# Performance work log

Hardware: AMD Instinct MI355X
Metric: run time of the kernel (lower is better)

The kernel has to match this reference:

```python
import jax, jax.numpy as jnp
import numpy as np

D_ENC = 512
D_DEC = 512
D_JOINT = D_ENC + D_DEC  # 1024
V = 1024


def setup_inputs() -> dict:
    key = jax.random.key(0)
    ks = jax.random.split(key, 8)
    s = lambda fan_in: 1.0 / np.sqrt(fan_in)
    return {
        "encoder_output": jax.random.normal(ks[0], (8, 200, D_ENC), dtype=jnp.float32),
        "decoder_output": jax.random.normal(ks[1], (8, 50, D_DEC), dtype=jnp.float32),
        "W_enc": jax.random.uniform(ks[2], (D_JOINT, D_ENC), jnp.float32, -s(D_ENC), s(D_ENC)),
        "b_enc": jax.random.uniform(ks[3], (D_JOINT,), jnp.float32, -s(D_ENC), s(D_ENC)),
        "W_dec": jax.random.uniform(ks[4], (D_JOINT, D_DEC), jnp.float32, -s(D_DEC), s(D_DEC)),
        "b_dec": jax.random.uniform(ks[5], (D_JOINT,), jnp.float32, -s(D_DEC), s(D_DEC)),
        "W_fc": jax.random.uniform(ks[6], (V, D_JOINT), jnp.float32, -s(D_JOINT), s(D_JOINT)),
        "b_fc": jax.random.uniform(ks[7], (V,), jnp.float32, -s(D_JOINT), s(D_JOINT)),
    }


def reference(encoder_output, decoder_output, W_enc, b_enc, W_dec, b_dec, W_fc, b_fc):
    # enc: (B, T, D_JOINT); dec: (B, U, D_JOINT)
    enc = jnp.einsum('btd,jd->btj', encoder_output, W_enc) + b_enc
    dec = jnp.einsum('bud,jd->buj', decoder_output, W_dec) + b_dec
    # broadcast join: (B, T, U, D_JOINT)
    combined = enc[:, :, None, :] + dec[:, None, :, :]
    logits = jnp.einsum('btuj,vj->btuv', jnp.tanh(combined), W_fc) + b_fc
    return jax.nn.log_softmax(logits, axis=-1)
```

## Files before the change

kernel.cpp:

```cpp
#include <hip/hip_runtime.h>
#include <hip/hip_bf16.h>

#define TT 200
#define UU 50
#define BB 8
#define DJ 1024
#define DE 512
#define VV 1024
#define M_TOTAL (BB*TT*UU)
#define MB 80
#define NITER 32

typedef __bf16 bf16x8 __attribute__((ext_vector_type(8)));
typedef float f32x4 __attribute__((ext_vector_type(4)));

__device__ __forceinline__ float fast_tanh(float x) {
    float e = __expf(2.f * x);
    return 1.f - 2.f / (e + 1.f);
}

__device__ __forceinline__ bf16x8 tanh_pack8(float4 e0, float4 e1, float4 d0, float4 d1) {
    bf16x8 h;
    h[0] = (__bf16)fast_tanh(e0.x + d0.x); h[1] = (__bf16)fast_tanh(e0.y + d0.y);
    h[2] = (__bf16)fast_tanh(e0.z + d0.z); h[3] = (__bf16)fast_tanh(e0.w + d0.w);
    h[4] = (__bf16)fast_tanh(e1.x + d1.x); h[5] = (__bf16)fast_tanh(e1.y + d1.y);
    h[6] = (__bf16)fast_tanh(e1.z + d1.z); h[7] = (__bf16)fast_tanh(e1.w + d1.w);
    return h;
}

__device__ __forceinline__ void gload_lds16(const unsigned short* g, unsigned short* l) {
    __builtin_amdgcn_global_load_lds(
        (const __attribute__((address_space(1))) unsigned int*)(const void*)g,
        (__attribute__((address_space(3))) unsigned int*)(void*)l, 16, 0, 0);
}

__global__ void k_wfct(const float* __restrict__ w, unsigned short* __restrict__ o) {
    const int G = blockIdx.x * 256 + threadIdx.x;
    const int gk = G >> 10, n = G & 1023;
    const float* src = w + (size_t)n * DJ + gk * 8;
    float4 a = *(const float4*)(src);
    float4 b = *(const float4*)(src + 4);
    bf16x8 h;
    h[0] = (__bf16)a.x; h[1] = (__bf16)a.y; h[2] = (__bf16)a.z; h[3] = (__bf16)a.w;
    h[4] = (__bf16)b.x; h[5] = (__bf16)b.y; h[6] = (__bf16)b.z; h[7] = (__bf16)b.w;
    *(bf16x8*)(o + (size_t)G * 8) = h;
}

__global__ __launch_bounds__(256) void k_proj2(const float* __restrict__ enc,
                                               const float* __restrict__ dec,
                                               const float* __restrict__ W_enc,
                                               const float* __restrict__ b_enc,
                                               const float* __restrict__ W_dec,
                                               const float* __restrict__ b_dec,
                                               float* __restrict__ encp,
                                               float* __restrict__ decp) {
    __shared__ float in_s[16][DE];
    const bool isDec = blockIdx.x >= 100;
    const float* in  = isDec ? dec   : enc;
    const float* W   = isDec ? W_dec : W_enc;
    const float* bia = isDec ? b_dec : b_enc;
    float* out       = isDec ? decp  : encp;
    const int m0 = (isDec ? (blockIdx.x - 100) : blockIdx.x) * 16;
    const int tid = threadIdx.x;
    #pragma unroll
    for (int it = 0; it < 8; ++it) {
        int idx = tid + it * 256;
        int r = idx >> 7, c = (idx & 127) << 2;
        *(float4*)&in_s[r][c] = *(const float4*)(in + (size_t)(m0 + r) * DE + c);
    }
    __syncthreads();
    const int j = blockIdx.y * 256 + tid;
    const float4* wr = (const float4*)(W + (size_t)j * DE);
    float acc[16];
    #pragma unroll
    for (int r = 0; r < 16; ++r) acc[r] = 0.f;
    for (int d4 = 0; d4 < DE / 4; ++d4) {
        float4 w = wr[d4];
        #pragma unroll
        for (int r = 0; r < 16; ++r) {
            float4 x = *(const float4*)&in_s[r][d4 << 2];
            acc[r] += x.x * w.x + x.y * w.y + x.z * w.z + x.w * w.w;
        }
    }
    float bv = bia[j];
    #pragma unroll
    for (int r = 0; r < 16; ++r)
        out[(size_t)(m0 + r) * DJ + j] = acc[r] + bv;
}

__global__ __launch_bounds__(512, 2) void k_joint(const float* __restrict__ encp,
                                                  const float* __restrict__ decp,
                                                  const unsigned short* __restrict__ wfcg,
                                                  const float* __restrict__ bfc,
                                                  float* __restrict__ out) {
    __shared__ unsigned short Bs[2][4096 * 8];
    __shared__ unsigned short As[2][320 * 8];
    __shared__ float red[8][MB];

    const int tid = threadIdx.x;
    const int wave = tid >> 6, lane = tid & 63;
    const int g = lane >> 4, ln = lane & 15;
    const int bid = blockIdx.x;
    const int m0 = bid * MB;

    const bool aRole = (tid < 320);
    const float *er = encp, *dr = decp;
    int agran = 0;
    if (aRole) {
        const int m = tid % MB;
        const int gk = tid / MB;
        const int mrow = m0 + m;
        const int b = mrow / (TT * UU);
        const int rem = mrow - b * (TT * UU);
        const int t = rem / UU;
        const int u = rem - t * UU;
        er = encp + (size_t)(b * TT + t) * DJ + gk * 8;
        dr = decp + (size_t)(b * UU + u) * DJ + gk * 8;
        agran = gk * MB + m;
    }

    f32x4 acc[5][8];
    #pragma unroll
    for (int mf = 0; mf < 5; ++mf)
        #pragma unroll
        for (int nf = 0; nf < 8; ++nf)
            acc[mf][nf] = (f32x4){0.f, 0.f, 0.f, 0.f};

    {
        const int kb0 = bid & 31;
        if (aRole) {
            const int ko = kb0 * 32;
            float4 e0 = *(const float4*)(er + ko);
            float4 e1 = *(const float4*)(er + ko + 4);
            float4 d0 = *(const float4*)(dr + ko);
            float4 d1 = *(const float4*)(dr + ko + 4);
            *(bf16x8*)&As[0][agran * 8] = tanh_pack8(e0, e1, d0, d1);
        }
        const unsigned short* src = wfcg + (size_t)kb0 * 4096 * 8;
        #pragma unroll
        for (int r = 0; r < 8; ++r)
            gload_lds16(src + (size_t)(r * 512 + tid) * 8, &Bs[0][(r * 512 + wave * 64) * 8]);
    }
    __syncthreads();

    for (int it = 0; it < NITER; ++it) {
        const int cur = it & 1, nxt = cur ^ 1;
        const bool notlast = (it < NITER - 1);
        float4 e0, e1, d0, d1;
        if (notlast) {
            const int kb = (it + 1 + bid) & 31;
            if (aRole) {
                const int ko = kb * 32;
                e0 = *(const float4*)(er + ko);
                e1 = *(const float4*)(er + ko + 4);
                d0 = *(const float4*)(dr + ko);
                d1 = *(const float4*)(dr + ko + 4);
            }
            const unsigned short* src = wfcg + (size_t)kb * 4096 * 8;
            #pragma unroll
            for (int r = 0; r < 8; ++r)
                gload_lds16(src + (size_t)(r * 512 + tid) * 8, &Bs[nxt][(r * 512 + wave * 64) * 8]);
        }
        bf16x8 af[5];
        #pragma unroll
        for (int mf = 0; mf < 5; ++mf)
            af[mf] = *(const bf16x8*)&As[cur][(g * MB + mf * 16 + ln) * 8];
        #pragma unroll
        for (int nf = 0; nf < 8; ++nf) {
            bf16x8 bfr = *(const bf16x8*)&Bs[cur][(g * 1024 + wave * 128 + nf * 16 + ln) * 8];
            #pragma unroll
            for (int mf = 0; mf < 5; ++mf)
                acc[mf][nf] = __builtin_amdgcn_mfma_f32_16x16x32_bf16(af[mf], bfr, acc[mf][nf], 0, 0, 0);
        }
        if (notlast && aRole)
            *(bf16x8*)&As[nxt][agran * 8] = tanh_pack8(e0, e1, d0, d1);
        __syncthreads();
    }

    float bv[8];
    #pragma unroll
    for (int nf = 0; nf < 8; ++nf) bv[nf] = bfc[wave * 128 + nf * 16 + ln];
    #pragma unroll
    for (int mf = 0; mf < 5; ++mf)
        #pragma unroll
        for (int nf = 0; nf < 8; ++nf)
            #pragma unroll
            for (int j = 0; j < 4; ++j)
                acc[mf][nf][j] += bv[nf];

    float rmx[5][4];
    #pragma unroll
    for (int mf = 0; mf < 5; ++mf)
        #pragma unroll
        for (int j = 0; j < 4; ++j) {
            float mx = -3.0e38f;
            #pragma unroll
            for (int nf = 0; nf < 8; ++nf) mx = fmaxf(mx, acc[mf][nf][j]);
            #pragma unroll
            for (int s = 1; s < 16; s <<= 1) mx = fmaxf(mx, __shfl_xor(mx, s));
            rmx[mf][j] = mx;
        }
    if (ln == 0) {
        #pragma unroll
        for (int mf = 0; mf < 5; ++mf)
            #pragma unroll
            for (int j = 0; j < 4; ++j)
                red[wave][mf * 16 + g * 4 + j] = rmx[mf][j];
    }
    __syncthreads();
    #pragma unroll
    for (int mf = 0; mf < 5; ++mf)
        #pragma unroll
        for (int j = 0; j < 4; ++j) {
            const int r = mf * 16 + g * 4 + j;
            float mx = red[0][r];
            #pragma unroll
            for (int w = 1; w < 8; ++w) mx = fmaxf(mx, red[w][r]);
            rmx[mf][j] = mx;
        }
    __syncthreads();

    float rsm[5][4];
    #pragma unroll
    for (int mf = 0; mf < 5; ++mf)
        #pragma unroll
        for (int j = 0; j < 4; ++j) {
            float s = 0.f;
            #pragma unroll
            for (int nf = 0; nf < 8; ++nf) s += __expf(acc[mf][nf][j] - rmx[mf][j]);
            #pragma unroll
            for (int t2 = 1; t2 < 16; t2 <<= 1) s += __shfl_xor(s, t2);
            rsm[mf][j] = s;
        }
    if (ln == 0) {
        #pragma unroll
        for (int mf = 0; mf < 5; ++mf)
            #pragma unroll
            for (int j = 0; j < 4; ++j)
                red[wave][mf * 16 + g * 4 + j] = rsm[mf][j];
    }
    __syncthreads();
    #pragma unroll
    for (int mf = 0; mf < 5; ++mf)
        #pragma unroll
        for (int j = 0; j < 4; ++j) {
            const int r = mf * 16 + g * 4 + j;
            float s = 0.f;
            #pragma unroll
            for (int w = 0; w < 8; ++w) s += red[w][r];
            const float lse = rmx[mf][j] + __logf(s);
            float* op = out + (size_t)(m0 + r) * VV + wave * 128 + ln;
            #pragma unroll
            for (int nf = 0; nf < 8; ++nf)
                __builtin_nontemporal_store(acc[mf][nf][j] - lse, op + nf * 16);
        }
}

extern "C" void kernel_launch(void* const* d_in, const int* in_sizes, int n_in,
                              void* d_out, int out_size, void* d_ws, size_t ws_size,
                              hipStream_t stream) {
    const float* enc   = (const float*)d_in[0];
    const float* dec   = (const float*)d_in[1];
    const float* W_enc = (const float*)d_in[2];
    const float* b_enc = (const float*)d_in[3];
    const float* W_dec = (const float*)d_in[4];
    const float* b_dec = (const float*)d_in[5];
    const float* W_fc  = (const float*)d_in[6];
    const float* b_fc  = (const float*)d_in[7];
    float* out = (float*)d_out;

    float* encp = (float*)d_ws;
    float* decp = encp + (size_t)BB * TT * DJ;
    unsigned short* wfcg = (unsigned short*)(decp + (size_t)BB * UU * DJ);

    k_wfct<<<(VV * DJ) / (256 * 8), 256, 0, stream>>>(W_fc, wfcg);
    k_proj2<<<dim3(125, DJ / 256), 256, 0, stream>>>(enc, dec, W_enc, b_enc, W_dec, b_dec, encp, decp);
    k_joint<<<M_TOTAL / MB, 512, 0, stream>>>(encp, decp, wfcg, b_fc, out);
}
```

Measured before the change: 404.1 us.

## Switch joint GEMM to FP8 MFMA with scaled weights and triple-buffered LDS

Converts the W_fc weights (pre-scaled by 32) and the tanh activations to FP8 e4m3, and runs the joint GEMM with fp8 MFMA instead of bf16. The scale is removed in the epilogue before the bias is added. This halves LDS and global traffic per K-step and uses the higher-rate FP8 matrix instructions. The double buffer becomes a three-stage LDS ring with manual s_waitcnt plus barrier, and the MFMA section runs at raised wave priority. The cost is lower precision in the logits, which may approach the accuracy tolerance.

```diff
diff --git a/kernel.cpp b/kernel.cpp
--- a/kernel.cpp
+++ b/kernel.cpp
@@ -1,5 +1,6 @@
 #include <hip/hip_runtime.h>
 #include <hip/hip_bf16.h>
+#include <hip/hip_fp8.h>
 
 #define TT 200
 #define UU 50
@@ -10,8 +11,8 @@
 #define M_TOTAL (BB*TT*UU)
 #define MB 80
 #define NITER 32
-
-typedef __bf16 bf16x8 __attribute__((ext_vector_type(8)));
+#define WINV (1.0f/32.0f)
+
 typedef float f32x4 __attribute__((ext_vector_type(4)));
 
 __device__ __forceinline__ float fast_tanh(float x) {
@@ -19,31 +20,45 @@
     return 1.f - 2.f / (e + 1.f);
 }
 
-__device__ __forceinline__ bf16x8 tanh_pack8(float4 e0, float4 e1, float4 d0, float4 d1) {
-    bf16x8 h;
-    h[0] = (__bf16)fast_tanh(e0.x + d0.x); h[1] = (__bf16)fast_tanh(e0.y + d0.y);
-    h[2] = (__bf16)fast_tanh(e0.z + d0.z); h[3] = (__bf16)fast_tanh(e0.w + d0.w);
-    h[4] = (__bf16)fast_tanh(e1.x + d1.x); h[5] = (__bf16)fast_tanh(e1.y + d1.y);
-    h[6] = (__bf16)fast_tanh(e1.z + d1.z); h[7] = (__bf16)fast_tanh(e1.w + d1.w);
-    return h;
-}
-
-__device__ __forceinline__ void gload_lds16(const unsigned short* g, unsigned short* l) {
+__device__ __forceinline__ unsigned char f2fp8(float x) {
+    return __hip_fp8_e4m3(x).__x;
+}
+
+__device__ __forceinline__ unsigned long long tanh_pack_fp8(float4 e0, float4 e1, float4 d0, float4 d1) {
+    unsigned long long r;
+    r  = (unsigned long long)f2fp8(fast_tanh(e0.x + d0.x));
+    r |= (unsigned long long)f2fp8(fast_tanh(e0.y + d0.y)) << 8;
+    r |= (unsigned long long)f2fp8(fast_tanh(e0.z + d0.z)) << 16;
+    r |= (unsigned long long)f2fp8(fast_tanh(e0.w + d0.w)) << 24;
+    r |= (unsigned long long)f2fp8(fast_tanh(e1.x + d1.x)) << 32;
+    r |= (unsigned long long)f2fp8(fast_tanh(e1.y + d1.y)) << 40;
+    r |= (unsigned long long)f2fp8(fast_tanh(e1.z + d1.z)) << 48;
+    r |= (unsigned long long)f2fp8(fast_tanh(e1.w + d1.w)) << 56;
+    return r;
+}
+
+__device__ __forceinline__ void gload_lds16(const unsigned char* g, unsigned char* l) {
     __builtin_amdgcn_global_load_lds(
         (const __attribute__((address_space(1))) unsigned int*)(const void*)g,
         (__attribute__((address_space(3))) unsigned int*)(void*)l, 16, 0, 0);
 }
 
-__global__ void k_wfct(const float* __restrict__ w, unsigned short* __restrict__ o) {
+__global__ void k_wfct(const float* __restrict__ w, unsigned char* __restrict__ o) {
     const int G = blockIdx.x * 256 + threadIdx.x;
     const int gk = G >> 10, n = G & 1023;
     const float* src = w + (size_t)n * DJ + gk * 8;
     float4 a = *(const float4*)(src);
     float4 b = *(const float4*)(src + 4);
-    bf16x8 h;
-    h[0] = (__bf16)a.x; h[1] = (__bf16)a.y; h[2] = (__bf16)a.z; h[3] = (__bf16)a.w;
-    h[4] = (__bf16)b.x; h[5] = (__bf16)b.y; h[6] = (__bf16)b.z; h[7] = (__bf16)b.w;
-    *(bf16x8*)(o + (size_t)G * 8) = h;
+    unsigned long long r;
+    r  = (unsigned long long)f2fp8(a.x * 32.f);
+    r |= (unsigned long long)f2fp8(a.y * 32.f) << 8;
+    r |= (unsigned long long)f2fp8(a.z * 32.f) << 16;
+    r |= (unsigned long long)f2fp8(a.w * 32.f) << 24;
+    r |= (unsigned long long)f2fp8(b.x * 32.f) << 32;
+    r |= (unsigned long long)f2fp8(b.y * 32.f) << 40;
+    r |= (unsigned long long)f2fp8(b.z * 32.f) << 48;
+    r |= (unsigned long long)f2fp8(b.w * 32.f) << 56;
+    *(unsigned long long*)(o + (size_t)G * 8) = r;
 }
 
 __global__ __launch_bounds__(256) void k_proj2(const float* __restrict__ enc,
@@ -90,11 +105,11 @@
 
 __global__ __launch_bounds__(512, 2) void k_joint(const float* __restrict__ encp,
                                                   const float* __restrict__ decp,
-                                                  const unsigned short* __restrict__ wfcg,
+                                                  const unsigned char* __restrict__ wfc8,
                                                   const float* __restrict__ bfc,
                                                   float* __restrict__ out) {
-    __shared__ unsigned short Bs[2][4096 * 8];
-    __shared__ unsigned short As[2][320 * 8];
+    __shared__ unsigned char Bs[3][32768];
+    __shared__ unsigned char As[3][2560];
     __shared__ float red[8][MB];
 
     const int tid = threadIdx.x;
@@ -127,54 +142,66 @@
             acc[mf][nf] = (f32x4){0.f, 0.f, 0.f, 0.f};
 
     {
-        const int kb0 = bid & 31;
+        const int kb0 = bid & 31, kb1 = (bid + 1) & 31;
+        float4 e0, e1, d0, d1;
         if (aRole) {
-            const int ko = kb0 * 32;
-            float4 e0 = *(const float4*)(er + ko);
-            float4 e1 = *(const float4*)(er + ko + 4);
-            float4 d0 = *(const float4*)(dr + ko);
-            float4 d1 = *(const float4*)(dr + ko + 4);
-            *(bf16x8*)&As[0][agran * 8] = tanh_pack8(e0, e1, d0, d1);
-        }
-        const unsigned short* src = wfcg + (size_t)kb0 * 4096 * 8;
-        #pragma unroll
-        for (int r = 0; r < 8; ++r)
-            gload_lds16(src + (size_t)(r * 512 + tid) * 8, &Bs[0][(r * 512 + wave * 64) * 8]);
-    }
-    __syncthreads();
-
-    for (int it = 0; it < NITER; ++it) {
-        const int cur = it & 1, nxt = cur ^ 1;
-        const bool notlast = (it < NITER - 1);
+            const int ko = kb0 << 5;
+            e0 = *(const float4*)(er + ko);
+            e1 = *(const float4*)(er + ko + 4);
+            d0 = *(const float4*)(dr + ko);
+            d1 = *(const float4*)(dr + ko + 4);
+        }
+        const unsigned char* s0 = wfc8 + (size_t)kb0 * 32768;
+        #pragma unroll
+        for (int r = 0; r < 4; ++r)
+            gload_lds16(s0 + (r * 512 + tid) * 16, &Bs[0][(r * 512 + tid) * 16]);
+        const unsigned char* s1 = wfc8 + (size_t)kb1 * 32768;
+        #pragma unroll
+        for (int r = 0; r < 4; ++r)
+            gload_lds16(s1 + (r * 512 + tid) * 16, &Bs[1][(r * 512 + tid) * 16]);
+        if (aRole)
+            *(unsigned long long*)&As[0][(size_t)agran * 8] = tanh_pack_fp8(e0, e1, d0, d1);
+    }
+
+    for (int t = 0; t < NITER; ++t) {
+        const int cb = t % 3;
+        if (t < NITER - 1)
+            asm volatile("s_waitcnt vmcnt(4) lgkmcnt(0)\n\ts_barrier" ::: "memory");
+        else
+            asm volatile("s_waitcnt vmcnt(0) lgkmcnt(0)\n\ts_barrier" ::: "memory");
+
         float4 e0, e1, d0, d1;
-        if (notlast) {
-            const int kb = (it + 1 + bid) & 31;
-            if (aRole) {
-                const int ko = kb * 32;
-                e0 = *(const float4*)(er + ko);
-                e1 = *(const float4*)(er + ko + 4);
-                d0 = *(const float4*)(dr + ko);
-                d1 = *(const float4*)(dr + ko + 4);
-            }
-            const unsigned short* src = wfcg + (size_t)kb * 4096 * 8;
-            #pragma unroll
-            for (int r = 0; r < 8; ++r)
-                gload_lds16(src + (size_t)(r * 512 + tid) * 8, &Bs[nxt][(r * 512 + wave * 64) * 8]);
-        }
-        bf16x8 af[5];
+        const bool haveA = aRole && (t < NITER - 1);
+        if (haveA) {
+            const int ko = ((t + 1 + bid) & 31) << 5;
+            e0 = *(const float4*)(er + ko);
+            e1 = *(const float4*)(er + ko + 4);
+            d0 = *(const float4*)(dr + ko);
+            d1 = *(const float4*)(dr + ko + 4);
+        }
+        if (t < NITER - 2) {
+            const unsigned char* src = wfc8 + (size_t)((t + 2 + bid) & 31) * 32768;
+            #pragma unroll
+            for (int r = 0; r < 4; ++r)
+                gload_lds16(src + (r * 512 + tid) * 16, &Bs[(t + 2) % 3][(r * 512 + tid) * 16]);
+        }
+
+        __builtin_amdgcn_s_setprio(1);
+        long afr[5];
         #pragma unroll
         for (int mf = 0; mf < 5; ++mf)
-            af[mf] = *(const bf16x8*)&As[cur][(g * MB + mf * 16 + ln) * 8];
+            afr[mf] = *(const long*)&As[cb][(size_t)(g * MB + mf * 16 + ln) * 8];
         #pragma unroll
         for (int nf = 0; nf < 8; ++nf) {
-            bf16x8 bfr = *(const bf16x8*)&Bs[cur][(g * 1024 + wave * 128 + nf * 16 + ln) * 8];
+            long bfr = *(const long*)&Bs[cb][(size_t)(g * 1024 + wave * 128 + nf * 16 + ln) * 8];
             #pragma unroll
             for (int mf = 0; mf < 5; ++mf)
-                acc[mf][nf] = __builtin_amdgcn_mfma_f32_16x16x32_bf16(af[mf], bfr, acc[mf][nf], 0, 0, 0);
-        }
-        if (notlast && aRole)
-            *(bf16x8*)&As[nxt][agran * 8] = tanh_pack8(e0, e1, d0, d1);
-        __syncthreads();
+                acc[mf][nf] = __builtin_amdgcn_mfma_f32_16x16x32_fp8_fp8(afr[mf], bfr, acc[mf][nf], 0, 0, 0);
+        }
+        __builtin_amdgcn_s_setprio(0);
+
+        if (haveA)
+            *(unsigned long long*)&As[(t + 1) % 3][(size_t)agran * 8] = tanh_pack_fp8(e0, e1, d0, d1);
     }
 
     float bv[8];
@@ -186,7 +213,7 @@
         for (int nf = 0; nf < 8; ++nf)
             #pragma unroll
             for (int j = 0; j < 4; ++j)
-                acc[mf][nf][j] += bv[nf];
+                acc[mf][nf][j] = acc[mf][nf][j] * WINV + bv[nf];
 
     float rmx[5][4];
     #pragma unroll
@@ -271,9 +298,9 @@
 
     float* encp = (float*)d_ws;
     float* decp = encp + (size_t)BB * TT * DJ;
-    unsigned short* wfcg = (unsigned short*)(decp + (size_t)BB * UU * DJ);
-
-    k_wfct<<<(VV * DJ) / (256 * 8), 256, 0, stream>>>(W_fc, wfcg);
+    unsigned char* wfc8 = (unsigned char*)(decp + (size_t)BB * UU * DJ);
+
+    k_wfct<<<(VV * DJ) / (256 * 8), 256, 0, stream>>>(W_fc, wfc8);
     k_proj2<<<dim3(125, DJ / 256), 256, 0, stream>>>(enc, dec, W_enc, b_enc, W_dec, b_dec, encp, decp);
-    k_joint<<<M_TOTAL / MB, 512, 0, stream>>>(encp, decp, wfcg, b_fc, out);
-}
+    k_joint<<<M_TOTAL / MB, 512, 0, stream>>>(encp, decp, wfc8, b_fc, out);
+}
```

Result: no change. 402.0 us (-0.5%).
